# Kernel tuning notes

Measured on AMD Instinct MI355X. Metric: run time of the kernel, lower is better.

## Reference

```python
import jax, jax.numpy as jnp
import numpy as np

NEUMANN_TERMS = 6
EPS_PASSTHROUGH = 1e-6  # hn_config.GRADIENT_PASSTHROUGH_EPSILON (assumed)


def _cayley_neumann(W, terms=NEUMANN_TERMS):
    """Cayley transform U = (I - A)^{-1} (I + A) with A = skew(W),
    where (I - A)^{-1} is approximated by the truncated Neumann series
    sum_{k=0}^{terms-1} A^k."""
    A = 0.5 * (W - W.T)                       # skew-symmetric generator
    I = jnp.eye(W.shape[0], dtype=W.dtype)
    S = I
    P = I
    for _ in range(terms - 1):                # small fixed loop (neumann_terms)
        P = P @ A
        S = S + P
    return S @ (I + A)


def _quantum_rotation(h, theta):
    """Parametric quantum rotation activation: rotate adjacent feature pairs
    by angle theta (norm-preserving, replaces ReLU/GELU)."""
    N, d = h.shape
    hp = h.reshape(N, d // 2, 2)
    c, s = jnp.cos(theta), jnp.sin(theta)
    x0, x1 = hp[..., 0], hp[..., 1]
    r0 = c * x0 - s * x1
    r1 = s * x0 + c * x1
    return jnp.stack([r0, r1], axis=-1).reshape(N, d)


def setup_inputs() -> dict:
    key = jax.random.key(0)
    k1, k2, k3 = jax.random.split(key, 3)
    N, d_model, d_ff = 65536, 1024, 1024
    inputs = jax.random.normal(k1, (N, d_model), dtype=jnp.float32)
    # Orthogonal initializer with gain 0.1 (as in build())
    q1 = jnp.linalg.qr(jax.random.normal(k2, (d_ff, d_model), dtype=jnp.float32))[0]
    q2 = jnp.linalg.qr(jax.random.normal(k3, (d_model, d_ff), dtype=jnp.float32))[0]
    u1_weights = 0.1 * q1
    u2_weights = 0.1 * q2
    activation_angle = jnp.float32(0.7854)  # pi/4 initializer
    return {"inputs": inputs, "u1_weights": u1_weights,
            "u2_weights": u2_weights, "activation_angle": activation_angle}


def reference(inputs, u1_weights, u2_weights, activation_angle):
    U1 = _cayley_neumann(u1_weights)          # [d_ff, d_model]
    U2 = _cayley_neumann(u2_weights)          # [d_model, d_ff]
    h = inputs @ U1.T                         # [N, d_ff]
    h = _quantum_rotation(h, activation_angle)
    out = h @ U2.T                            # [N, d_model]
    # gradient passthrough term from call()
    passthrough = (jnp.mean(u1_weights) * EPS_PASSTHROUGH
                   + jnp.mean(u2_weights) * EPS_PASSTHROUGH
                   + activation_angle * EPS_PASSTHROUGH)
    return out + passthrough
```

## Files before the change

### kernel.cpp

```cpp
#include <hip/hip_runtime.h>
#include <hip/hip_bf16.h>
#include <stdint.h>


#define MM (1024 * 1024)

typedef __attribute__((ext_vector_type(4))) float f32x4;
typedef __attribute__((ext_vector_type(8))) short bf16x8;

__device__ __forceinline__ ushort f2bf(float f) {
  uint32_t u = __builtin_bit_cast(uint32_t, f);
  u += 0x7FFFu + ((u >> 16) & 1u);
  return (ushort)(u >> 16);
}
__device__ __forceinline__ float bf2f(ushort h) {
  uint32_t u = ((uint32_t)h) << 16;
  return __builtin_bit_cast(float, u);
}

__device__ __forceinline__ void gld_lds16(const ushort* g, ushort* l) {
  __builtin_amdgcn_global_load_lds(
      (const __attribute__((address_space(1))) unsigned int*)g,
      (__attribute__((address_space(3))) unsigned int*)l, 16, 0, 0);
}

__global__ __launch_bounds__(256, 2) void gemm_bt(
    const ushort* __restrict__ X0, const ushort* __restrict__ X1,
    const ushort* __restrict__ Y0, const ushort* __restrict__ Y1,
    float* __restrict__ o32, ushort* __restrict__ o16,
    ushort* __restrict__ o16b, const float* __restrict__ aux,
    int M, int N, int K, int mode,
    const float* __restrict__ theta_p, const float* __restrict__ sums) {
  __shared__ ushort lA[128 * 32];
  __shared__ ushort lB[128 * 32];

  const int tid = threadIdx.x;
  const int wave = tid >> 6, lane = tid & 63;
  const int bz = blockIdx.z;
  const int job = bz >> 1, mi = bz & 1;

  const int nwg = gridDim.x * gridDim.y;
  const int lin = blockIdx.y * gridDim.x + blockIdx.x;
  const int swz = (lin & 7) * (nwg >> 3) + (lin >> 3);
  const int bn = swz & 7;
  const int bm = swz >> 3;

  const ushort* X = (job ? X1 : X0) + (size_t)mi * MM;
  const ushort* Y = (job ? Y1 : Y0) + (size_t)mi * MM;

  const ushort* Xg = X + (size_t)(bm * 128 + (tid >> 2)) * K + (tid & 3) * 8;
  const ushort* Yg = Y + (size_t)(bn * 128 + (tid >> 2)) * K + (tid & 3) * 8;
  ushort* lAw = lA + wave * 512;
  ushort* lBw = lB + wave * 512;

  const int wm = (wave & 1) * 64;
  const int wn = (wave >> 1) * 64;
  const int lr = lane & 15;
  const int kq = (lane >> 4) * 8;

  f32x4 acc[4][4] = {};

  for (int k0 = 0; k0 < K; k0 += 32) {
    __syncthreads();
    gld_lds16(Xg + k0, lAw);
    gld_lds16(Xg + k0 + (size_t)64 * K, lAw + 64 * 32);
    gld_lds16(Yg + k0, lBw);
    gld_lds16(Yg + k0 + (size_t)64 * K, lBw + 64 * 32);
    __syncthreads();

    bf16x8 af[4], bfg[4];
#pragma unroll
    for (int t = 0; t < 4; ++t) {
      af[t] = *(const bf16x8*)(lA + (wm + t * 16 + lr) * 32 + kq);
      bfg[t] = *(const bf16x8*)(lB + (wn + t * 16 + lr) * 32 + kq);
    }
#pragma unroll
    for (int ti = 0; ti < 4; ++ti)
#pragma unroll
      for (int tj = 0; tj < 4; ++tj)
        acc[ti][tj] = __builtin_amdgcn_mfma_f32_16x16x32_bf16(
            af[ti], bfg[tj], acc[ti][tj], 0, 0, 0);
  }

  const int q4 = (lane >> 4) * 4;
  if (mode == 1) {
    float th = *theta_p, s, c;
    __sincosf(th, &s, &c);
    const float ssgn = (lane & 1) ? s : -s;
#pragma unroll
    for (int ti = 0; ti < 4; ++ti)
#pragma unroll
      for (int r = 0; r < 4; ++r) {
        size_t row = (size_t)(bm * 128 + wm + ti * 16 + q4 + r);
        ushort* Orow = o16 + row * N;
#pragma unroll
        for (int tj = 0; tj < 4; ++tj) {
          float v = acc[ti][tj][r];
          float w = __shfl_xor(v, 1);
          Orow[bn * 128 + wn + tj * 16 + lr] = f2bf(c * v + ssgn * w);
        }
      }
  } else if (mode == 2) {
    const float pt = 1e-6f * (sums[0] * (1.0f / 1048576.0f) +
                              sums[1] * (1.0f / 1048576.0f) + *theta_p);
#pragma unroll
    for (int ti = 0; ti < 4; ++ti)
#pragma unroll
      for (int r = 0; r < 4; ++r) {
        size_t row = (size_t)(bm * 128 + wm + ti * 16 + q4 + r);
        float* Orow = o32 + row * N;
#pragma unroll
        for (int tj = 0; tj < 4; ++tj)
          Orow[bn * 128 + wn + tj * 16 + lr] = acc[ti][tj][r] + pt;
      }
  } else {
    float* O = o32 + (size_t)bz * MM;
    ushort* P0 = (mode >= 3) ? o16 + (size_t)bz * MM : nullptr;
    ushort* P1 = (mode == 4) ? o16b + (size_t)bz * MM : nullptr;
    const float* Ax = (mode == 4) ? aux + (size_t)bz * MM : nullptr;
#pragma unroll
    for (int ti = 0; ti < 4; ++ti)
#pragma unroll
      for (int r = 0; r < 4; ++r) {
        const int row = bm * 128 + wm + ti * 16 + q4 + r;
        const size_t base = (size_t)row * N;
#pragma unroll
        for (int tj = 0; tj < 4; ++tj) {
          const int col = bn * 128 + wn + tj * 16 + lr;
          const float v = acc[ti][tj][r];
          O[base + col] = v;
          if (mode == 3) {
            P0[base + col] = f2bf(-v);
          } else if (mode == 4) {
            P0[base + col] = f2bf(v);
            const float diag = (row == col) ? 1.f : 0.f;
            P1[base + col] = f2bf(diag - Ax[base + col] + v);
          }
        }
      }
  }
}

__global__ __launch_bounds__(256) void prep_a(const float* __restrict__ W1,
                                              const float* __restrict__ W2,
                                              ushort* __restrict__ Abf,
                                              float* __restrict__ sums) {
  __shared__ float sT[32][33];
  const int z = blockIdx.z;
  const float* W = z ? W2 : W1;
  ushort* A = Abf + (size_t)z * MM;
  const int r0 = blockIdx.y * 32, c0 = blockIdx.x * 32;
  const int x = threadIdx.x, y = threadIdx.y;

#pragma unroll
  for (int k = 0; k < 4; ++k)
    sT[y + 8 * k][x] = W[(size_t)(c0 + y + 8 * k) * 1024 + r0 + x];
  __syncthreads();

  float lsum = 0.f;
#pragma unroll
  for (int k = 0; k < 4; ++k) {
    int i = y + 8 * k;
    float w = W[(size_t)(r0 + i) * 1024 + c0 + x];
    lsum += w;
    A[(size_t)(r0 + i) * 1024 + c0 + x] = f2bf(0.5f * (w - sT[x][i]));
  }
#pragma unroll
  for (int off = 32; off > 0; off >>= 1) lsum += __shfl_down(lsum, off);
  if (((y * 32 + x) & 63) == 0) atomicAdd(&sums[z], lsum);
}

__global__ __launch_bounds__(256) void cvt_x(const float* __restrict__ x,
                                             ushort* __restrict__ xb) {
  const size_t i = (size_t)blockIdx.x * 256 + threadIdx.x;
  float4 v = ((const float4*)x)[i];
  ushort4 o;
  o.x = f2bf(v.x);
  o.y = f2bf(v.y);
  o.z = f2bf(v.z);
  o.w = f2bf(v.w);
  ((ushort4*)xb)[i] = o;
}

__global__ __launch_bounds__(256) void ew(const float* __restrict__ S1,
                                          const float* __restrict__ S2,
                                          const float* __restrict__ S3,
                                          const float* __restrict__ S4,
                                          ushort* __restrict__ O0) {
  const int idx = blockIdx.x * 256 + threadIdx.x;
  const int local = idx & (MM - 1);
  const float diag = ((local >> 10) == (local & 1023)) ? 1.f : 0.f;
  O0[idx] =
      f2bf(diag - 2.f * S1[idx] + 2.f * S2[idx] + 2.f * S3[idx] + S4[idx]);
}

extern "C" void kernel_launch(void* const* d_in, const int* in_sizes, int n_in,
                              void* d_out, int out_size, void* d_ws,
                              size_t ws_size, hipStream_t stream) {
  const float* xin = (const float*)d_in[0];
  const float* w1 = (const float*)d_in[1];
  const float* w2 = (const float*)d_in[2];
  const float* th = (const float*)d_in[3];
  float* out = (float*)d_out;

  char* w = (char*)d_ws;
  float* sums = (float*)w;
  ushort* Abf = (ushort*)(w + 256);
  ushort* Bbf = Abf + 2 * MM;
  ushort* B2bf = Bbf + 2 * MM;
  ushort* Fbf = B2bf + 2 * MM;
  ushort* Ubf = Fbf + 2 * MM;
  float* S1 = (float*)(Ubf + 2 * MM);
  float* S2 = S1 + 2 * MM;
  float* S34 = S2 + 2 * MM;
  ushort* xbf = (ushort*)(S34 + 4 * MM);
  ushort* hbf = xbf + (size_t)65536 * 1024;

  hipMemsetAsync(sums, 0, 2 * sizeof(float), stream);

  prep_a<<<dim3(32, 32, 2), dim3(32, 8), 0, stream>>>(w1, w2, Abf, sums);
  cvt_x<<<65536, 256, 0, stream>>>(xin, xbf);

  gemm_bt<<<dim3(8, 8, 2), 256, 0, stream>>>(Abf, Abf, Abf, Abf, S1, Bbf,
                                             nullptr, nullptr, 1024, 1024,
                                             1024, 3, th, sums);
  gemm_bt<<<dim3(8, 8, 2), 256, 0, stream>>>(Bbf, Bbf, Bbf, Bbf, S2, B2bf,
                                             Fbf, S1, 1024, 1024, 1024, 4, th,
                                             sums);
  gemm_bt<<<dim3(8, 8, 4), 256, 0, stream>>>(Abf, B2bf, Fbf, Bbf, S34, nullptr,
                                             nullptr, nullptr, 1024, 1024,
                                             1024, 0, th, sums);
  ew<<<8192, 256, 0, stream>>>(S1, S2, S34, S34 + 2 * MM, Ubf);

  gemm_bt<<<dim3(8, 512, 1), 256, 0, stream>>>(xbf, xbf, Ubf, Ubf, nullptr,
                                               hbf, nullptr, nullptr, 65536,
                                               1024, 1024, 1, th, sums);
  gemm_bt<<<dim3(8, 512, 1), 256, 0, stream>>>(hbf, hbf, Ubf + MM, Ubf + MM,
                                               out, nullptr, nullptr, nullptr,
                                               65536, 1024, 1024, 2, th, sums);
}
```

Before: 972.0 us.

## Add double-buffered 256x256 GEMM kernel with swizzled LDS for large matmuls

Adds a new gemm256 kernel for the two large N=65536 GEMMs. It uses 512 threads, 256x256 output tiles and a K-tile of 64 with double-buffered LDS (128KB dynamic). Global-to-LDS prefetch is interleaved with MFMA phases using raw barriers and setprio, and the LDS layout is XOR-swizzled to avoid bank conflicts. The aim is more data reuse per tile and hiding of load latency behind compute. The cost is much higher LDS and register pressure, which may limit occupancy, plus hand-managed vmcnt waits that must be correct.

```diff
diff --git a/kernel.cpp b/kernel.cpp
--- a/kernel.cpp
+++ b/kernel.cpp
@@ -13,10 +13,6 @@
   u += 0x7FFFu + ((u >> 16) & 1u);
   return (ushort)(u >> 16);
 }
-__device__ __forceinline__ float bf2f(ushort h) {
-  uint32_t u = ((uint32_t)h) << 16;
-  return __builtin_bit_cast(float, u);
-}
 
 __device__ __forceinline__ void gld_lds16(const ushort* g, ushort* l) {
   __builtin_amdgcn_global_load_lds(
@@ -24,13 +20,171 @@
       (__attribute__((address_space(3))) unsigned int*)l, 16, 0, 0);
 }
 
+#define STAGE(GS, LB, BUF, H, KT)                                    \
+  do {                                                               \
+    const ushort* g_ = (GS) + (size_t)((H)*128) * K + (size_t)(KT)*64; \
+    ushort* d_ = (LB) + (BUF)*32768 + (H)*128 * 64;                  \
+    gld_lds16(g_, d_);                                               \
+    gld_lds16(g_ + (size_t)64 * K, d_ + 64 * 64);                    \
+  } while (0)
+
+#define LDA(MH, BUF)                                                    \
+  do {                                                                  \
+    _Pragma("unroll") for (int ti = 0; ti < 4; ++ti) {                  \
+      const ushort* p_ = rdA + (BUF)*32768 + ((MH)*64 + ti * 16 + lr) * 64; \
+      af[ti][0] = *(const bf16x8*)(p_ + (pcol0 >> 1));                  \
+      af[ti][1] = *(const bf16x8*)(p_ + (pcol1 >> 1));                  \
+    }                                                                   \
+  } while (0)
+
+#define LDB(NH, BUF)                                                    \
+  do {                                                                  \
+    _Pragma("unroll") for (int tj = 0; tj < 2; ++tj) {                  \
+      const ushort* p_ = rdB + (BUF)*32768 + ((NH)*32 + tj * 16 + lr) * 64; \
+      bfr[tj][0] = *(const bf16x8*)(p_ + (pcol0 >> 1));                 \
+      bfr[tj][1] = *(const bf16x8*)(p_ + (pcol1 >> 1));                 \
+    }                                                                   \
+  } while (0)
+
+#define MFMA16(MH, NH)                                                  \
+  do {                                                                  \
+    __builtin_amdgcn_s_setprio(1);                                      \
+    _Pragma("unroll") for (int m_ = 0; m_ < 4; ++m_)                    \
+    _Pragma("unroll") for (int n_ = 0; n_ < 2; ++n_)                    \
+    _Pragma("unroll") for (int ks_ = 0; ks_ < 2; ++ks_)                 \
+      acc[(MH)*4 + m_][(NH)*2 + n_] =                                   \
+          __builtin_amdgcn_mfma_f32_16x16x32_bf16(                      \
+              af[m_][ks_], bfr[n_][ks_], acc[(MH)*4 + m_][(NH)*2 + n_], \
+              0, 0, 0);                                                 \
+    __builtin_amdgcn_s_setprio(0);                                      \
+  } while (0)
+
+#define CFENCE asm volatile("" ::: "memory")
+#define SBAR                                  \
+  do {                                        \
+    CFENCE;                                   \
+    __builtin_amdgcn_s_barrier();             \
+    __builtin_amdgcn_sched_barrier(0);        \
+  } while (0)
+
+__global__ __launch_bounds__(512, 2) void gemm256(
+    const ushort* __restrict__ X, const ushort* __restrict__ Y,
+    float* __restrict__ o32, ushort* __restrict__ o16, int M, int N, int K,
+    int mode, const float* __restrict__ theta_p,
+    const float* __restrict__ sums) {
+  extern __shared__ ushort lds[];
+
+  const int tid = threadIdx.x;
+  const int wave = tid >> 6, lane = tid & 63;
+
+  const int nwg = gridDim.x * gridDim.y;
+  const int lin = blockIdx.y * gridDim.x + blockIdx.x;
+  const int wgid = (lin & 7) * (nwg >> 3) + (lin >> 3);
+  const int bn = wgid & 3;
+  const int bm = wgid >> 2;
+
+  const int wrow = wave >> 2;
+  const int wcol = wave & 3;
+
+  const int srow = wave * 8 + (lane >> 3);
+  const int scol = (((lane & 7) ^ ((lane >> 3) & 7)) << 3);
+  const ushort* Xs = X + (size_t)(bm * 256 + srow) * K + scol;
+  const ushort* Ys = Y + (size_t)(bn * 256 + srow) * K + scol;
+  ushort* stA = lds + wave * 8 * 64;
+  ushort* stB = lds + 16384 + wave * 8 * 64;
+
+  const int lr = lane & 15;
+  const int kqb = (lane >> 4) << 4;
+  const int swz = (lr & 7) << 4;
+  const int pcol0 = (0 + kqb) ^ swz;
+  const int pcol1 = (64 + kqb) ^ swz;
+  const ushort* rdA = lds + wrow * 128 * 64;
+  const ushort* rdB = lds + 16384 + wcol * 64 * 64;
+
+  f32x4 acc[8][4] = {};
+  bf16x8 af[4][2], bfr[2][2];
+
+  const int NT = K >> 6;
+
+  STAGE(Xs, stA, 0, 0, 0);
+  STAGE(Xs, stA, 0, 1, 0);
+  STAGE(Ys, stB, 0, 0, 0);
+  STAGE(Ys, stB, 0, 1, 0);
+
+  for (int t = 0; t < NT; ++t) {
+    const int cur = t & 1, nxt = cur ^ 1;
+    const bool pf = (t + 1 < NT);
+    if (pf) {
+      STAGE(Xs, stA, nxt, 0, t + 1);
+      asm volatile("s_waitcnt vmcnt(2)" ::: "memory");
+    } else {
+      asm volatile("s_waitcnt vmcnt(0)" ::: "memory");
+    }
+    SBAR;
+    LDA(0, cur);
+    LDB(0, cur);
+    MFMA16(0, 0);
+    SBAR;
+    LDB(1, cur);
+    if (pf) STAGE(Xs, stA, nxt, 1, t + 1);
+    SBAR;
+    MFMA16(0, 1);
+    SBAR;
+    LDA(1, cur);
+    if (pf) STAGE(Ys, stB, nxt, 0, t + 1);
+    SBAR;
+    MFMA16(1, 1);
+    SBAR;
+    LDB(0, cur);
+    if (pf) STAGE(Ys, stB, nxt, 1, t + 1);
+    SBAR;
+    MFMA16(1, 0);
+    SBAR;
+  }
+
+  const int q4 = (lane >> 4) * 4;
+  const int rbase = bm * 256 + wrow * 128;
+  const int cbase = bn * 256 + wcol * 64;
+  if (mode == 1) {
+    float th = *theta_p, s, c;
+    __sincosf(th, &s, &c);
+    const float ssgn = (lane & 1) ? s : -s;
+#pragma unroll
+    for (int fi = 0; fi < 8; ++fi)
+#pragma unroll
+      for (int r = 0; r < 4; ++r) {
+        const size_t row = (size_t)(rbase + fi * 16 + q4 + r);
+        ushort* Orow = o16 + row * N;
+#pragma unroll
+        for (int fj = 0; fj < 4; ++fj) {
+          float v = acc[fi][fj][r];
+          float w = __shfl_xor(v, 1);
+          Orow[cbase + fj * 16 + lr] = f2bf(c * v + ssgn * w);
+        }
+      }
+  } else {
+    const float pt = 1e-6f * (sums[0] * (1.0f / 1048576.0f) +
+                              sums[1] * (1.0f / 1048576.0f) + *theta_p);
+#pragma unroll
+    for (int fi = 0; fi < 8; ++fi)
+#pragma unroll
+      for (int r = 0; r < 4; ++r) {
+        const size_t row = (size_t)(rbase + fi * 16 + q4 + r);
+        float* Orow = o32 + row * N;
+#pragma unroll
+        for (int fj = 0; fj < 4; ++fj)
+          Orow[cbase + fj * 16 + lr] = acc[fi][fj][r] + pt;
+      }
+  }
+}
+
 __global__ __launch_bounds__(256, 2) void gemm_bt(
     const ushort* __restrict__ X0, const ushort* __restrict__ X1,
     const ushort* __restrict__ Y0, const ushort* __restrict__ Y1,
     float* __restrict__ o32, ushort* __restrict__ o16,
-    ushort* __restrict__ o16b, const float* __restrict__ aux,
-    int M, int N, int K, int mode,
-    const float* __restrict__ theta_p, const float* __restrict__ sums) {
+    ushort* __restrict__ o16b, const float* __restrict__ aux, int M, int N,
+    int K, int mode, const float* __restrict__ theta_p,
+    const float* __restrict__ sums) {
   __shared__ ushort lA[128 * 32];
   __shared__ ushort lB[128 * 32];
 
@@ -41,9 +195,9 @@
 
   const int nwg = gridDim.x * gridDim.y;
   const int lin = blockIdx.y * gridDim.x + blockIdx.x;
-  const int swz = (lin & 7) * (nwg >> 3) + (lin >> 3);
-  const int bn = swz & 7;
-  const int bm = swz >> 3;
+  const int swzb = (lin & 7) * (nwg >> 3) + (lin >> 3);
+  const int bn = swzb & 7;
+  const int bm = swzb >> 3;
 
   const ushort* X = (job ? X1 : X0) + (size_t)mi * MM;
   const ushort* Y = (job ? Y1 : Y0) + (size_t)mi * MM;
@@ -68,10 +222,10 @@
     gld_lds16(Yg + k0 + (size_t)64 * K, lBw + 64 * 32);
     __syncthreads();
 
-    bf16x8 af[4], bfg[4];
+    bf16x8 afv[4], bfg[4];
 #pragma unroll
     for (int t = 0; t < 4; ++t) {
-      af[t] = *(const bf16x8*)(lA + (wm + t * 16 + lr) * 32 + kq);
+      afv[t] = *(const bf16x8*)(lA + (wm + t * 16 + lr) * 32 + kq);
       bfg[t] = *(const bf16x8*)(lB + (wn + t * 16 + lr) * 32 + kq);
     }
 #pragma unroll
@@ -79,66 +233,34 @@
 #pragma unroll
       for (int tj = 0; tj < 4; ++tj)
         acc[ti][tj] = __builtin_amdgcn_mfma_f32_16x16x32_bf16(
-            af[ti], bfg[tj], acc[ti][tj], 0, 0, 0);
+            afv[ti], bfg[tj], acc[ti][tj], 0, 0, 0);
   }
 
   const int q4 = (lane >> 4) * 4;
-  if (mode == 1) {
-    float th = *theta_p, s, c;
-    __sincosf(th, &s, &c);
-    const float ssgn = (lane & 1) ? s : -s;
-#pragma unroll
-    for (int ti = 0; ti < 4; ++ti)
-#pragma unroll
-      for (int r = 0; r < 4; ++r) {
-        size_t row = (size_t)(bm * 128 + wm + ti * 16 + q4 + r);
-        ushort* Orow = o16 + row * N;
-#pragma unroll
-        for (int tj = 0; tj < 4; ++tj) {
-          float v = acc[ti][tj][r];
-          float w = __shfl_xor(v, 1);
-          Orow[bn * 128 + wn + tj * 16 + lr] = f2bf(c * v + ssgn * w);
+  float* O = o32 + (size_t)bz * MM;
+  ushort* P0 = (mode >= 3) ? o16 + (size_t)bz * MM : nullptr;
+  ushort* P1 = (mode == 4) ? o16b + (size_t)bz * MM : nullptr;
+  const float* Ax = (mode == 4) ? aux + (size_t)bz * MM : nullptr;
+#pragma unroll
+  for (int ti = 0; ti < 4; ++ti)
+#pragma unroll
+    for (int r = 0; r < 4; ++r) {
+      const int row = bm * 128 + wm + ti * 16 + q4 + r;
+      const size_t base = (size_t)row * N;
+#pragma unroll
+      for (int tj = 0; tj < 4; ++tj) {
+        const int col = bn * 128 + wn + tj * 16 + lr;
+        const float v = acc[ti][tj][r];
+        O[base + col] = v;
+        if (mode == 3) {
+          P0[base + col] = f2bf(-v);
+        } else if (mode == 4) {
+          P0[base + col] = f2bf(v);
+          const float diag = (row == col) ? 1.f : 0.f;
+          P1[base + col] = f2bf(diag - Ax[base + col] + v);
         }
       }
-  } else if (mode == 2) {
-    const float pt = 1e-6f * (sums[0] * (1.0f / 1048576.0f) +
-                              sums[1] * (1.0f / 1048576.0f) + *theta_p);
-#pragma unroll
-    for (int ti = 0; ti < 4; ++ti)
-#pragma unroll
-      for (int r = 0; r < 4; ++r) {
-        size_t row = (size_t)(bm * 128 + wm + ti * 16 + q4 + r);
-        float* Orow = o32 + row * N;
-#pragma unroll
-        for (int tj = 0; tj < 4; ++tj)
-          Orow[bn * 128 + wn + tj * 16 + lr] = acc[ti][tj][r] + pt;
-      }
-  } else {
-    float* O = o32 + (size_t)bz * MM;
-    ushort* P0 = (mode >= 3) ? o16 + (size_t)bz * MM : nullptr;
-    ushort* P1 = (mode == 4) ? o16b + (size_t)bz * MM : nullptr;
-    const float* Ax = (mode == 4) ? aux + (size_t)bz * MM : nullptr;
-#pragma unroll
-    for (int ti = 0; ti < 4; ++ti)
-#pragma unroll
-      for (int r = 0; r < 4; ++r) {
-        const int row = bm * 128 + wm + ti * 16 + q4 + r;
-        const size_t base = (size_t)row * N;
-#pragma unroll
-        for (int tj = 0; tj < 4; ++tj) {
-          const int col = bn * 128 + wn + tj * 16 + lr;
-          const float v = acc[ti][tj][r];
-          O[base + col] = v;
-          if (mode == 3) {
-            P0[base + col] = f2bf(-v);
-          } else if (mode == 4) {
-            P0[base + col] = f2bf(v);
-            const float diag = (row == col) ? 1.f : 0.f;
-            P1[base + col] = f2bf(diag - Ax[base + col] + v);
-          }
-        }
-      }
-  }
+    }
 }
 
 __global__ __launch_bounds__(256) void prep_a(const float* __restrict__ W1,
@@ -216,6 +338,14 @@
   ushort* xbf = (ushort*)(S34 + 4 * MM);
   ushort* hbf = xbf + (size_t)65536 * 1024;
 
+  static bool inited = false;
+  if (!inited) {
+    (void)hipFuncSetAttribute((const void*)gemm256,
+                              hipFuncAttributeMaxDynamicSharedMemorySize,
+                              131072);
+    inited = true;
+  }
+
   hipMemsetAsync(sums, 0, 2 * sizeof(float), stream);
 
   prep_a<<<dim3(32, 32, 2), dim3(32, 8), 0, stream>>>(w1, w2, Abf, sums);
@@ -224,18 +354,16 @@
   gemm_bt<<<dim3(8, 8, 2), 256, 0, stream>>>(Abf, Abf, Abf, Abf, S1, Bbf,
                                              nullptr, nullptr, 1024, 1024,
                                              1024, 3, th, sums);
-  gemm_bt<<<dim3(8, 8, 2), 256, 0, stream>>>(Bbf, Bbf, Bbf, Bbf, S2, B2bf,
-                                             Fbf, S1, 1024, 1024, 1024, 4, th,
+  gemm_bt<<<dim3(8, 8, 2), 256, 0, stream>>>(Bbf, Bbf, Bbf, Bbf, S2, B2bf, Fbf,
+                                             S1, 1024, 1024, 1024, 4, th,
                                              sums);
   gemm_bt<<<dim3(8, 8, 4), 256, 0, stream>>>(Abf, B2bf, Fbf, Bbf, S34, nullptr,
                                              nullptr, nullptr, 1024, 1024,
                                              1024, 0, th, sums);
   ew<<<8192, 256, 0, stream>>>(S1, S2, S34, S34 + 2 * MM, Ubf);
 
-  gemm_bt<<<dim3(8, 512, 1), 256, 0, stream>>>(xbf, xbf, Ubf, Ubf, nullptr,
-                                               hbf, nullptr, nullptr, 65536,
-                                               1024, 1024, 1, th, sums);
-  gemm_bt<<<dim3(8, 512, 1), 256, 0, stream>>>(hbf, hbf, Ubf + MM, Ubf + MM,
-                                               out, nullptr, nullptr, nullptr,
-                                               65536, 1024, 1024, 2, th, sums);
-}
+  gemm256<<<dim3(4, 256, 1), 512, 131072, stream>>>(
+      xbf, Ubf, nullptr, hbf, 65536, 1024, 1024, 1, th, sums);
+  gemm256<<<dim3(4, 256, 1), 512, 131072, stream>>>(
+      hbf, Ubf + MM, out, nullptr, 65536, 1024, 1024, 2, th, sums);
+}
```

Result: faster. 913.6 us (-6.0%).
